# Optimization experiments

Measured on AMD Instinct MI355X. Metric: run time of the kernel, lower is better.

Reference implementation:

```python
import jax, jax.numpy as jnp
import numpy as np

H = 8            # num_heads
EPS = 1e-5       # LayerNorm eps (torch default)
SLOPE = 0.01     # leaky_relu negative slope (torch default)


def layernorm(x, g, b):
    mu = jnp.mean(x, axis=-1, keepdims=True)
    var = jnp.mean((x - mu) ** 2, axis=-1, keepdims=True)
    return (x - mu) * jax.lax.rsqrt(var + EPS) * g + b


def setup_inputs() -> dict:
    key = jax.random.key(0)
    ks = jax.random.split(key, 20)
    B, T, Din, Dh = 4, 2048, 512, 512
    s_in = 1.0 / np.sqrt(Din)
    s_h = 1.0 / np.sqrt(Dh)
    inp = {
        'q': jax.random.normal(ks[0], (B, T, Din), jnp.float32),
        'k': jax.random.normal(ks[1], (B, T, Din), jnp.float32),
        'v': jax.random.normal(ks[2], (B, T, Din), jnp.float32),
        # attention projections (stored as [in, out] for x @ W + b)
        'Wq': jax.random.uniform(ks[3], (Din, Dh), jnp.float32, -s_in, s_in),
        'bq': jax.random.uniform(ks[4], (Dh,), jnp.float32, -s_in, s_in),
        'Wk': jax.random.uniform(ks[5], (Din, Dh), jnp.float32, -s_in, s_in),
        'bk': jax.random.uniform(ks[6], (Dh,), jnp.float32, -s_in, s_in),
        'Wv': jax.random.uniform(ks[7], (Din, Dh), jnp.float32, -s_in, s_in),
        'bv': jax.random.uniform(ks[8], (Dh,), jnp.float32, -s_in, s_in),
        'Wo': jax.random.uniform(ks[9], (Dh, Dh), jnp.float32, -s_h, s_h),
        'bo': jax.random.uniform(ks[10], (Dh,), jnp.float32, -s_h, s_h),
        # FFN
        'Wh': jax.random.uniform(ks[11], (Dh, Dh), jnp.float32, -s_h, s_h),
        'bh': jax.random.uniform(ks[12], (Dh,), jnp.float32, -s_h, s_h),
        'W2': jax.random.uniform(ks[13], (Dh, Dh), jnp.float32, -s_h, s_h),
        'b2': jax.random.uniform(ks[14], (Dh,), jnp.float32, -s_h, s_h),
        # LayerNorms
        'g1': jnp.ones((Dh,), jnp.float32),
        'be1': jnp.zeros((Dh,), jnp.float32),
        'g2': jnp.ones((Dh,), jnp.float32),
        'be2': jnp.zeros((Dh,), jnp.float32),
    }
    return inp


def _block(q, k, v, Wq, bq, Wk, bk, Wv, bv, Wo, bo, Wh, bh, W2, b2, g1, be1, g2, be2):
    B, Tq, _ = q.shape
    Tk = k.shape[1]
    Dh = Wq.shape[1]
    dh = Dh // H
    # projections -> [B, H, T, dh]
    qh = (q @ Wq + bq).reshape(B, Tq, H, dh).transpose(0, 2, 1, 3)
    kh = (k @ Wk + bk).reshape(B, Tk, H, dh).transpose(0, 2, 1, 3)
    vh = (v @ Wv + bv).reshape(B, Tk, H, dh).transpose(0, 2, 1, 3)
    scores = jnp.einsum('bhqd,bhkd->bhqk', qh, kh) / np.sqrt(dh)
    # causal mask: tril with diagonal = Tk - Tq (matches get_causal_mask)
    mask = jnp.tril(jnp.ones((Tq, Tk), bool), k=Tk - Tq)
    scores = jnp.where(mask, scores, -jnp.inf)
    attn = jax.nn.softmax(scores, axis=-1)
    x = jnp.einsum('bhqk,bhkd->bhqd', attn, vh)
    x = x.transpose(0, 2, 1, 3).reshape(B, Tq, Dh)
    h = x @ Wo + bo
    if h.shape == q.shape:
        h = h + q  # residual
    h = layernorm(h, g1, be1)
    y = jax.nn.leaky_relu(h @ Wh + bh, SLOPE) @ W2 + b2
    y = y + h  # residual (shapes always equal here)
    return layernorm(y, g2, be2)


def reference(q, k, v, Wq, bq, Wk, bk, Wv, bv, Wo, bo, Wh, bh, W2, b2, g1, be1, g2, be2):
    return _block(q, k, v, Wq, bq, Wk, bk, Wv, bv, Wo, bo, Wh, bh, W2, b2, g1, be1, g2, be2)
```

## Files before the change

kernel.cpp:

```cpp
#include <hip/hip_runtime.h>
#include <math.h>

#define DIN   512
#define TSEQ  2048
#define BATCH 4
#define NH    8
#define DHEAD 64
#define MTOT  8192

typedef __attribute__((ext_vector_type(8))) __bf16 bf16x8;
typedef __attribute__((ext_vector_type(8))) short  s16x8;
typedef __attribute__((ext_vector_type(4))) float  f32x4;

__device__ __forceinline__ unsigned short f2b(float f) {
  union { float f; unsigned int u; } c; c.f = f;
  unsigned int r = (c.u + 0x7fffu + ((c.u >> 16) & 1u)) >> 16;
  return (unsigned short)r;
}

__device__ __forceinline__ unsigned int pkbf(float a, float b) {
  union { __bf16 h[2]; unsigned int u; } c;
  c.h[0] = (__bf16)a; c.h[1] = (__bf16)b; return c.u;
}

__device__ __forceinline__ f32x4 mfma16(bf16x8 a, bf16x8 b, f32x4 c) {
  return __builtin_amdgcn_mfma_f32_16x16x32_bf16(a, b, c, 0, 0, 0);
}

__device__ __forceinline__ void gload16(const void* gsrc, void* ldsbase) {
  __builtin_amdgcn_global_load_lds(
      (const __attribute__((address_space(1))) unsigned int*)gsrc,
      (__attribute__((address_space(3))) unsigned int*)(unsigned int)(unsigned long long)ldsbase,
      16, 0, 0);
}

#define VMCNT0_BARRIER() do { \
    asm volatile("s_waitcnt vmcnt(0)" ::: "memory"); \
    __builtin_amdgcn_s_barrier(); } while (0)

__global__ __launch_bounds__(256) void cast3_kernel(const float* __restrict__ q,
                                                    const float* __restrict__ k,
                                                    const float* __restrict__ v,
                                                    unsigned short* __restrict__ oq,
                                                    unsigned short* __restrict__ ok,
                                                    unsigned short* __restrict__ ov) {
  const float* in = blockIdx.y == 0 ? q : blockIdx.y == 1 ? k : v;
  unsigned short* out = blockIdx.y == 0 ? oq : blockIdx.y == 1 ? ok : ov;
  int i = (blockIdx.x * 256 + threadIdx.x) * 8;
  float4 a = *(const float4*)(in + i);
  float4 b = *(const float4*)(in + i + 4);
  ushort4 u0, u1;
  u0.x = f2b(a.x); u0.y = f2b(a.y); u0.z = f2b(a.z); u0.w = f2b(a.w);
  u1.x = f2b(b.x); u1.y = f2b(b.y); u1.z = f2b(b.z); u1.w = f2b(b.w);
  *(ushort4*)(out + i) = u0;
  *(ushort4*)(out + i + 4) = u1;
}

__global__ __launch_bounds__(256) void transpose6_kernel(const float* __restrict__ w0,
                                                         const float* __restrict__ w1,
                                                         const float* __restrict__ w2,
                                                         const float* __restrict__ w3,
                                                         const float* __restrict__ w4,
                                                         const float* __restrict__ w5,
                                                         unsigned short* __restrict__ Wt) {
  const float* W;
  switch (blockIdx.z) {
    case 0: W = w0; break; case 1: W = w1; break; case 2: W = w2; break;
    case 3: W = w3; break; case 4: W = w4; break; default: W = w5; break;
  }
  unsigned short* dst = Wt + (size_t)blockIdx.z * 512 * 512;
  __shared__ float tile[32][33];
  int bx = blockIdx.x * 32, by = blockIdx.y * 32;
  int tx = threadIdx.x & 31, ty = threadIdx.x >> 5;
  #pragma unroll
  for (int yy = ty; yy < 32; yy += 8)
    tile[yy][tx] = W[(size_t)(by + yy) * DIN + bx + tx];
  __syncthreads();
  #pragma unroll
  for (int yy = ty; yy < 32; yy += 8)
    dst[(size_t)(bx + yy) * DIN + by + tx] = f2b(tile[tx][yy]);
}

__device__ __forceinline__ void gemm_core(const unsigned short* __restrict__ A,
                                          const unsigned short* __restrict__ Bt,
                                          int m0, int n0,
                                          unsigned short (*Als)[64 * 64],
                                          unsigned short (*Bls)[128 * 64],
                                          f32x4 (*acc)[4]) {
  const int tid = threadIdx.x, lane = tid & 63, w = tid >> 6;
  const int wr = w >> 1, wc = w & 1;
  const int l = lane & 15, g = lane >> 4;
  const int r8 = lane >> 3;
  const int sce = ((lane & 7) ^ r8) * 8;
  const int sxr = (l & 7) * 8;

  #define GSTAGE(buf, k0) do { \
      _Pragma("unroll") \
      for (int i_ = 0; i_ < 2; ++i_) { \
        int ia_ = w * 2 + i_; \
        gload16(A + (size_t)(m0 + ia_ * 8 + r8) * 512 + (k0) + sce, &Als[buf][ia_ * 512]); \
      } \
      _Pragma("unroll") \
      for (int i_ = 0; i_ < 4; ++i_) { \
        int ib_ = w * 4 + i_; \
        gload16(Bt + (size_t)(n0 + ib_ * 8 + r8) * 512 + (k0) + sce, &Bls[buf][ib_ * 512]); \
      } } while (0)

  GSTAGE(0, 0);
  VMCNT0_BARRIER();
  for (int t = 0; t < 8; ++t) {
    int cur = t & 1;
    if (t < 7) GSTAGE(cur ^ 1, (t + 1) * 64);
    #pragma unroll
    for (int kk = 0; kk < 2; ++kk) {
      bf16x8 af[2], bf[4];
      #pragma unroll
      for (int m = 0; m < 2; ++m)
        af[m] = *(const bf16x8*)(&Als[cur][(wr * 32 + m * 16 + l) * 64 + ((kk * 32 + g * 8) ^ sxr)]);
      #pragma unroll
      for (int n = 0; n < 4; ++n)
        bf[n] = *(const bf16x8*)(&Bls[cur][(wc * 64 + n * 16 + l) * 64 + ((kk * 32 + g * 8) ^ sxr)]);
      #pragma unroll
      for (int m = 0; m < 2; ++m)
        #pragma unroll
        for (int n = 0; n < 4; ++n)
          acc[m][n] = mfma16(af[m], bf[n], acc[m][n]);
    }
    VMCNT0_BARRIER();
  }
  #undef GSTAGE
}

enum { EPI_BF16 = 0, EPI_F32RES = 2, EPI_LRELU = 3 };

template <int EPI>
__global__ __launch_bounds__(256) void gemm_kernel(const unsigned short* __restrict__ A,
                                                   const unsigned short* __restrict__ Bt,
                                                   const float* __restrict__ bias,
                                                   const float* __restrict__ res,
                                                   void* __restrict__ out) {
  __shared__ unsigned short Als[2][64 * 64];
  __shared__ unsigned short Bls[2][128 * 64];
  const int lane = threadIdx.x & 63, w = threadIdx.x >> 6;
  const int wr = w >> 1, wc = w & 1;
  const int l = lane & 15, g = lane >> 4;
  const int m0 = blockIdx.x * 64, n0 = blockIdx.y * 128;
  f32x4 acc[2][4] = {};
  gemm_core(A, Bt, m0, n0, Als, Bls, acc);

  #pragma unroll
  for (int m = 0; m < 2; ++m) {
    int grb = m0 + wr * 32 + m * 16 + g * 4;
    #pragma unroll
    for (int n = 0; n < 4; ++n) {
      int gc = n0 + wc * 64 + n * 16 + l;
      float bv = bias[gc];
      #pragma unroll
      for (int r = 0; r < 4; ++r) {
        int gr = grb + r;
        float v = acc[m][n][r] + bv;
        if (EPI == EPI_F32RES) {
          ((float*)out)[(size_t)gr * 512 + gc] = v + res[(size_t)gr * 512 + gc];
        } else if (EPI == EPI_BF16) {
          ((unsigned short*)out)[(size_t)gr * 512 + gc] = f2b(v);
        } else {
          v = v > 0.f ? v : 0.01f * v;
          ((unsigned short*)out)[(size_t)gr * 512 + gc] = f2b(v);
        }
      }
    }
  }
}

__global__ __launch_bounds__(256) void gemm_qkv_kernel(const unsigned short* __restrict__ qb,
                                                       const unsigned short* __restrict__ kb,
                                                       const unsigned short* __restrict__ vb,
                                                       const unsigned short* __restrict__ Wt,
                                                       const float* __restrict__ bq,
                                                       const float* __restrict__ bk,
                                                       const float* __restrict__ bv,
                                                       unsigned short* __restrict__ Qp,
                                                       unsigned short* __restrict__ Kp,
                                                       unsigned short* __restrict__ Vt) {
  __shared__ unsigned short Als[2][64 * 64];
  __shared__ unsigned short Bls[2][128 * 64];
  const int z = blockIdx.z;
  const unsigned short* A = z == 0 ? qb : z == 1 ? kb : vb;
  const unsigned short* B = Wt + (size_t)z * 512 * 512;
  const float* bias = z == 0 ? bq : z == 1 ? bk : bv;
  const int lane = threadIdx.x & 63, w = threadIdx.x >> 6;
  const int wr = w >> 1, wc = w & 1;
  const int l = lane & 15, g = lane >> 4;
  const int m0 = blockIdx.x * 64, n0 = blockIdx.y * 128;
  f32x4 acc[2][4] = {};
  gemm_core(A, B, m0, n0, Als, Bls, acc);

  #pragma unroll
  for (int m = 0; m < 2; ++m) {
    int grb = m0 + wr * 32 + m * 16 + g * 4;
    #pragma unroll
    for (int n = 0; n < 4; ++n) {
      int gc = n0 + wc * 64 + n * 16 + l;
      float bvl = bias[gc];
      #pragma unroll
      for (int r = 0; r < 4; ++r) {
        int gr = grb + r;
        float v = acc[m][n][r] + bvl;
        if (z == 0) {
          Qp[(size_t)gr * 512 + gc] = f2b(v);
        } else if (z == 1) {
          Kp[(size_t)gr * 512 + gc] = f2b(v);
        } else {
          int b = gr >> 11, t = gr & 2047;
          Vt[((size_t)(b * 512 + gc) << 11) + t] = f2b(v);
        }
      }
    }
  }
}

__global__ __launch_bounds__(256) void attn_kernel(const unsigned short* __restrict__ Q,
                                                   const unsigned short* __restrict__ K,
                                                   const unsigned short* __restrict__ Vt,
                                                   unsigned short* __restrict__ O) {
  __shared__ unsigned short Kls[2][64 * 64];
  __shared__ unsigned short Vls[2][64 * 64];
  __shared__ unsigned short Pls[4][16 * 64];
  const int tid = threadIdx.x, lane = tid & 63, w = tid >> 6;
  const int l = lane & 15, g = lane >> 4;
  const int j = blockIdx.x;
  const int bh = blockIdx.y;
  const int b = bh >> 3, h = bh & 7;
  const int sx = (l & 7) * 8;
  const int n1 = 32 - j;
  const float SC2 = 0.125f * 1.44269504088896340736f;
  const float THR = 64.f;

  const int r8 = lane >> 3;
  const int sce = ((lane & 7) ^ r8) * 8;

  #define STAGEKV(buf, kv0) do { \
      _Pragma("unroll") \
      for (int i_ = 0; i_ < 2; ++i_) { \
        int ii_ = w * 2 + i_; \
        int row_ = ii_ * 8 + r8; \
        gload16(K  + (size_t)(b * 2048 + (kv0) + row_) * 512 + h * 64 + sce, &Kls[buf][ii_ * 512]); \
        gload16(Vt + (size_t)(b * 512 + h * 64 + row_) * 2048 + (kv0) + sce, &Vls[buf][ii_ * 512]); \
      } } while (0)

  int tile = 31 - j;
  int q0 = tile * 64 + w * 16;
  bf16x8 qf[2];
  #pragma unroll
  for (int kf = 0; kf < 2; ++kf)
    qf[kf] = *(const bf16x8*)(Q + (size_t)(b * 2048 + q0 + l) * 512 + h * 64 + kf * 32 + g * 8);

  float mrun = -1e30f, lrun = 0.f;
  f32x4 o[4] = {};

  STAGEKV(0, 0);
  VMCNT0_BARRIER();

  for (int s = 0; s <= 32; ++s) {
    int cur = s & 1;
    int kb = s < n1 ? s : s - n1;
    int kv0 = kb * 64;
    if (s < 32) {
      int kbn = (s + 1) < n1 ? (s + 1) : (s + 1) - n1;
      STAGEKV(cur ^ 1, kbn * 64);
    }

    f32x4 st[4];
    #pragma unroll
    for (int t = 0; t < 4; ++t) {
      st[t] = f32x4{0.f, 0.f, 0.f, 0.f};
      #pragma unroll
      for (int kf = 0; kf < 2; ++kf) {
        bf16x8 kfr = *(const bf16x8*)(&Kls[cur][(t * 16 + l) * 64 + ((kf * 32 + g * 8) ^ sx)]);
        st[t] = mfma16(kfr, qf[kf], st[t]);
      }
    }
    if (kb == tile) {
      const int qrow = q0 + l;
      #pragma unroll
      for (int t = 0; t < 4; ++t)
        #pragma unroll
        for (int r = 0; r < 4; ++r)
          if (kv0 + t * 16 + g * 4 + r > qrow) st[t][r] = -1e30f;
    }

    float mx = fmaxf(fmaxf(fmaxf(st[0][0], st[0][1]), fmaxf(st[0][2], st[0][3])),
                     fmaxf(fmaxf(st[1][0], st[1][1]), fmaxf(st[1][2], st[1][3])));
    mx = fmaxf(mx, fmaxf(fmaxf(fmaxf(st[2][0], st[2][1]), fmaxf(st[2][2], st[2][3])),
                         fmaxf(fmaxf(st[3][0], st[3][1]), fmaxf(st[3][2], st[3][3]))));
    mx = fmaxf(mx, __shfl_xor(mx, 16, 64));
    mx = fmaxf(mx, __shfl_xor(mx, 32, 64));

    if (!__all(mx <= mrun + THR)) {
      float nm = fmaxf(mrun, mx);
      float alpha = exp2f((mrun - nm) * SC2);
      mrun = nm;
      lrun *= alpha;
      #pragma unroll
      for (int r = 0; r < 4; ++r) {
        float ar = __shfl(alpha, g * 4 + r, 64);
        #pragma unroll
        for (int n = 0; n < 4; ++n) o[n][r] *= ar;
      }
    }

    float mS = mrun * SC2;
    float rs = 0.f;
    #pragma unroll
    for (int t = 0; t < 4; ++t)
      #pragma unroll
      for (int r = 0; r < 4; ++r) {
        float p = exp2f(fmaf(st[t][r], SC2, -mS));
        st[t][r] = p;
        rs += p;
      }
    rs += __shfl_xor(rs, 16, 64);
    rs += __shfl_xor(rs, 32, 64);
    lrun += rs;

    #pragma unroll
    for (int t = 0; t < 4; ++t) {
      uint2 u;
      u.x = pkbf(st[t][0], st[t][1]);
      u.y = pkbf(st[t][2], st[t][3]);
      *(uint2*)(&Pls[w][l * 64 + ((t * 16 + g * 4) ^ sx)]) = u;
    }
    #pragma unroll
    for (int kf = 0; kf < 2; ++kf) {
      bf16x8 pa = *(const bf16x8*)(&Pls[w][l * 64 + ((kf * 32 + g * 8) ^ sx)]);
      #pragma unroll
      for (int n = 0; n < 4; ++n) {
        bf16x8 vf = *(const bf16x8*)(&Vls[cur][(n * 16 + l) * 64 + ((kf * 32 + g * 8) ^ sx)]);
        o[n] = mfma16(pa, vf, o[n]);
      }
    }

    if (s == n1 - 1) {
      float li = 1.f / lrun;
      #pragma unroll
      for (int r = 0; r < 4; ++r) {
        float lir = __shfl(li, g * 4 + r, 64);
        #pragma unroll
        for (int n = 0; n < 4; ++n)
          O[(size_t)(b * 2048 + q0 + g * 4 + r) * 512 + h * 64 + n * 16 + l] =
              f2b(o[n][r] * lir);
      }
      tile = j;
      q0 = tile * 64 + w * 16;
      #pragma unroll
      for (int kf = 0; kf < 2; ++kf)
        qf[kf] = *(const bf16x8*)(Q + (size_t)(b * 2048 + q0 + l) * 512 + h * 64 + kf * 32 + g * 8);
      mrun = -1e30f; lrun = 0.f;
      #pragma unroll
      for (int n = 0; n < 4; ++n) o[n] = f32x4{0.f, 0.f, 0.f, 0.f};
    }
    VMCNT0_BARRIER();
  }

  float li = 1.f / lrun;
  #pragma unroll
  for (int r = 0; r < 4; ++r) {
    float lir = __shfl(li, g * 4 + r, 64);
    #pragma unroll
    for (int n = 0; n < 4; ++n)
      O[(size_t)(b * 2048 + q0 + g * 4 + r) * 512 + h * 64 + n * 16 + l] =
          f2b(o[n][r] * lir);
  }
  #undef STAGEKV
}

template <int WRITE_BF16>
__global__ __launch_bounds__(256) void ln_kernel(const float* __restrict__ X,
                                                 const float* __restrict__ g,
                                                 const float* __restrict__ be,
                                                 float* __restrict__ Yf,
                                                 unsigned short* __restrict__ Yb) {
  int row = blockIdx.x * 4 + (threadIdx.x >> 6);
  int lane = threadIdx.x & 63;
  const float* x = X + (size_t)row * 512;
  float4 v0 = *(const float4*)(x + lane * 4);
  float4 v1 = *(const float4*)(x + 256 + lane * 4);
  float s = v0.x + v0.y + v0.z + v0.w + v1.x + v1.y + v1.z + v1.w;
  #pragma unroll
  for (int t = 1; t < 64; t <<= 1) s += __shfl_xor(s, t, 64);
  float mu = s * (1.f / 512.f);
  float q = 0.f;
  q += (v0.x - mu) * (v0.x - mu); q += (v0.y - mu) * (v0.y - mu);
  q += (v0.z - mu) * (v0.z - mu); q += (v0.w - mu) * (v0.w - mu);
  q += (v1.x - mu) * (v1.x - mu); q += (v1.y - mu) * (v1.y - mu);
  q += (v1.z - mu) * (v1.z - mu); q += (v1.w - mu) * (v1.w - mu);
  #pragma unroll
  for (int t = 1; t < 64; t <<= 1) q += __shfl_xor(q, t, 64);
  float rstd = rsqrtf(q * (1.f / 512.f) + 1e-5f);

  float4 g0 = *(const float4*)(g + lane * 4);
  float4 g1 = *(const float4*)(g + 256 + lane * 4);
  float4 b0 = *(const float4*)(be + lane * 4);
  float4 b1 = *(const float4*)(be + 256 + lane * 4);
  float4 y0, y1;
  y0.x = (v0.x - mu) * rstd * g0.x + b0.x; y0.y = (v0.y - mu) * rstd * g0.y + b0.y;
  y0.z = (v0.z - mu) * rstd * g0.z + b0.z; y0.w = (v0.w - mu) * rstd * g0.w + b0.w;
  y1.x = (v1.x - mu) * rstd * g1.x + b1.x; y1.y = (v1.y - mu) * rstd * g1.y + b1.y;
  y1.z = (v1.z - mu) * rstd * g1.z + b1.z; y1.w = (v1.w - mu) * rstd * g1.w + b1.w;
  if (Yf) {
    *(float4*)(Yf + (size_t)row * 512 + lane * 4) = y0;
    *(float4*)(Yf + (size_t)row * 512 + 256 + lane * 4) = y1;
  }
  if (WRITE_BF16) {
    ushort4 u0, u1;
    u0.x = f2b(y0.x); u0.y = f2b(y0.y); u0.z = f2b(y0.z); u0.w = f2b(y0.w);
    u1.x = f2b(y1.x); u1.y = f2b(y1.y); u1.z = f2b(y1.z); u1.w = f2b(y1.w);
    *(ushort4*)(Yb + (size_t)row * 512 + lane * 4) = u0;
    *(ushort4*)(Yb + (size_t)row * 512 + 256 + lane * 4) = u1;
  }
}

extern "C" void kernel_launch(void* const* d_in, const int* in_sizes, int n_in,
                              void* d_out, int out_size, void* d_ws, size_t ws_size,
                              hipStream_t stream) {
  const float* q_in = (const float*)d_in[0];
  const float* k_in = (const float*)d_in[1];
  const float* v_in = (const float*)d_in[2];
  const float* Wq = (const float*)d_in[3];  const float* bq = (const float*)d_in[4];
  const float* Wk = (const float*)d_in[5];  const float* bk = (const float*)d_in[6];
  const float* Wv = (const float*)d_in[7];  const float* bv = (const float*)d_in[8];
  const float* Wo = (const float*)d_in[9];  const float* bo = (const float*)d_in[10];
  const float* Wh = (const float*)d_in[11]; const float* bh = (const float*)d_in[12];
  const float* W2 = (const float*)d_in[13]; const float* b2 = (const float*)d_in[14];
  const float* g1 = (const float*)d_in[15]; const float* be1 = (const float*)d_in[16];
  const float* g2 = (const float*)d_in[17]; const float* be2 = (const float*)d_in[18];

  char* ws = (char*)d_ws;
  const size_t MD2 = (size_t)MTOT * 512 * 2;
  const size_t W1  = (size_t)512 * 512 * 2;
  const size_t MD4 = (size_t)MTOT * 512 * 4;
  unsigned short* qb_  = (unsigned short*)(ws);
  unsigned short* kb_  = (unsigned short*)(ws + MD2);
  unsigned short* vb_  = (unsigned short*)(ws + 2 * MD2);
  unsigned short* Qp   = (unsigned short*)(ws + 3 * MD2);
  unsigned short* Kp   = (unsigned short*)(ws + 4 * MD2);
  unsigned short* Vt   = (unsigned short*)(ws + 5 * MD2);
  unsigned short* Wt   = (unsigned short*)(ws + 6 * MD2);
  float*          hy   = (float*)(ws + 6 * MD2 + 6 * W1);
  float*          ln1f = (float*)(ws + 6 * MD2 + 6 * W1 + MD4);
  unsigned short* attn = vb_;
  unsigned short* ln1b = qb_;
  unsigned short* f1   = kb_;

  cast3_kernel<<<dim3(MTOT * 512 / 2048, 3), 256, 0, stream>>>(q_in, k_in, v_in, qb_, kb_, vb_);
  transpose6_kernel<<<dim3(16, 16, 6), 256, 0, stream>>>(Wq, Wk, Wv, Wo, Wh, W2, Wt);

  gemm_qkv_kernel<<<dim3(MTOT / 64, 4, 3), 256, 0, stream>>>(
      qb_, kb_, vb_, Wt, bq, bk, bv, Qp, Kp, Vt);

  attn_kernel<<<dim3(16, BATCH * NH), 256, 0, stream>>>(Qp, Kp, Vt, attn);

  dim3 gg(MTOT / 64, 4);
  gemm_kernel<EPI_F32RES><<<gg, 256, 0, stream>>>(attn, Wt + 3 * 512 * 512, bo, q_in, hy);
  ln_kernel<1><<<MTOT / 4, 256, 0, stream>>>(hy, g1, be1, ln1f, ln1b);
  gemm_kernel<EPI_LRELU><<<gg, 256, 0, stream>>>(ln1b, Wt + 4 * 512 * 512, bh, nullptr, f1);
  gemm_kernel<EPI_F32RES><<<gg, 256, 0, stream>>>(f1, Wt + 5 * 512 * 512, b2, ln1f, hy);
  ln_kernel<0><<<MTOT / 4, 256, 0, stream>>>(hy, g2, be2, (float*)d_out, nullptr);
}
```

Baseline: 258.9 us.

## Triple-buffer LDS staging with vmcnt-based waits in GEMM and attention kernels

```diff
diff --git a/kernel.cpp b/kernel.cpp
--- a/kernel.cpp
+++ b/kernel.cpp
@@ -34,9 +34,7 @@
       16, 0, 0);
 }
 
-#define VMCNT0_BARRIER() do { \
-    asm volatile("s_waitcnt vmcnt(0)" ::: "memory"); \
-    __builtin_amdgcn_s_barrier(); } while (0)
+#define WAITV(N) asm volatile("s_waitcnt vmcnt(" #N ")" ::: "memory")
 
 __global__ __launch_bounds__(256) void cast3_kernel(const float* __restrict__ q,
                                                     const float* __restrict__ k,
@@ -107,10 +105,15 @@
       } } while (0)
 
   GSTAGE(0, 0);
-  VMCNT0_BARRIER();
+  GSTAGE(1, 64);
+  int cur = 0;
   for (int t = 0; t < 8; ++t) {
-    int cur = t & 1;
-    if (t < 7) GSTAGE(cur ^ 1, (t + 1) * 64);
+    if (t < 7) { WAITV(6); } else { WAITV(0); }
+    __builtin_amdgcn_s_barrier();
+    if (t < 6) {
+      int nb = cur + 2; if (nb >= 3) nb -= 3;
+      GSTAGE(nb, (t + 2) * 64);
+    }
     #pragma unroll
     for (int kk = 0; kk < 2; ++kk) {
       bf16x8 af[2], bf[4];
@@ -126,7 +129,7 @@
         for (int n = 0; n < 4; ++n)
           acc[m][n] = mfma16(af[m], bf[n], acc[m][n]);
     }
-    VMCNT0_BARRIER();
+    cur = cur == 2 ? 0 : cur + 1;
   }
   #undef GSTAGE
 }
@@ -139,8 +142,8 @@
                                                    const float* __restrict__ bias,
                                                    const float* __restrict__ res,
                                                    void* __restrict__ out) {
-  __shared__ unsigned short Als[2][64 * 64];
-  __shared__ unsigned short Bls[2][128 * 64];
+  __shared__ unsigned short Als[3][64 * 64];
+  __shared__ unsigned short Bls[3][128 * 64];
   const int lane = threadIdx.x & 63, w = threadIdx.x >> 6;
   const int wr = w >> 1, wc = w & 1;
   const int l = lane & 15, g = lane >> 4;
@@ -182,8 +185,8 @@
                                                        unsigned short* __restrict__ Qp,
                                                        unsigned short* __restrict__ Kp,
                                                        unsigned short* __restrict__ Vt) {
-  __shared__ unsigned short Als[2][64 * 64];
-  __shared__ unsigned short Bls[2][128 * 64];
+  __shared__ unsigned short Als[3][64 * 64];
+  __shared__ unsigned short Bls[3][128 * 64];
   const int z = blockIdx.z;
   const unsigned short* A = z == 0 ? qb : z == 1 ? kb : vb;
   const unsigned short* B = Wt + (size_t)z * 512 * 512;
@@ -223,13 +226,13 @@
                                                    const unsigned short* __restrict__ K,
                                                    const unsigned short* __restrict__ Vt,
                                                    unsigned short* __restrict__ O) {
-  __shared__ unsigned short Kls[2][64 * 64];
-  __shared__ unsigned short Vls[2][64 * 64];
+  __shared__ unsigned short Kls[3][64 * 64];
+  __shared__ unsigned short Vls[3][64 * 64];
   __shared__ unsigned short Pls[4][16 * 64];
   const int tid = threadIdx.x, lane = tid & 63, w = tid >> 6;
   const int l = lane & 15, g = lane >> 4;
-  const int j = blockIdx.x;
-  const int bh = blockIdx.y;
+  const int j = blockIdx.y;
+  const int bh = blockIdx.x;
   const int b = bh >> 3, h = bh & 7;
   const int sx = (l & 7) * 8;
   const int n1 = 32 - j;
@@ -259,16 +262,20 @@
   f32x4 o[4] = {};
 
   STAGEKV(0, 0);
-  VMCNT0_BARRIER();
+  STAGEKV(1, 64);
+  int cur = 0;
 
   for (int s = 0; s <= 32; ++s) {
-    int cur = s & 1;
+    if (s < 32) { WAITV(4); } else { WAITV(0); }
+    __builtin_amdgcn_s_barrier();
+    if (s + 2 <= 32) {
+      int sp = s + 2;
+      int kbp = sp < n1 ? sp : sp - n1;
+      int nb = cur + 2; if (nb >= 3) nb -= 3;
+      STAGEKV(nb, kbp * 64);
+    }
     int kb = s < n1 ? s : s - n1;
     int kv0 = kb * 64;
-    if (s < 32) {
-      int kbn = (s + 1) < n1 ? (s + 1) : (s + 1) - n1;
-      STAGEKV(cur ^ 1, kbn * 64);
-    }
 
     f32x4 st[4];
     #pragma unroll
@@ -359,7 +366,7 @@
       #pragma unroll
       for (int n = 0; n < 4; ++n) o[n] = f32x4{0.f, 0.f, 0.f, 0.f};
     }
-    VMCNT0_BARRIER();
+    cur = cur == 2 ? 0 : cur + 1;
   }
 
   float li = 1.f / lrun;
@@ -458,7 +465,7 @@
   gemm_qkv_kernel<<<dim3(MTOT / 64, 4, 3), 256, 0, stream>>>(
       qb_, kb_, vb_, Wt, bq, bk, bv, Qp, Kp, Vt);
 
-  attn_kernel<<<dim3(16, BATCH * NH), 256, 0, stream>>>(Qp, Kp, Vt, attn);
+  attn_kernel<<<dim3(BATCH * NH, 16), 256, 0, stream>>>(Qp, Kp, Vt, attn);
 
   dim3 gg(MTOT / 64, 4);
   gemm_kernel<EPI_F32RES><<<gg, 256, 0, stream>>>(attn, Wt + 3 * 512 * 512, bo, q_in, hy);
```

After: 256.1 us. No clear change (-1.1%).

## Launch one attention block per query tile and compute softmax row sums via MFMA

Applied to the files above, without the earlier changes.

```diff
diff --git a/kernel.cpp b/kernel.cpp
--- a/kernel.cpp
+++ b/kernel.cpp
@@ -228,11 +228,10 @@
   __shared__ unsigned short Pls[4][16 * 64];
   const int tid = threadIdx.x, lane = tid & 63, w = tid >> 6;
   const int l = lane & 15, g = lane >> 4;
-  const int j = blockIdx.x;
-  const int bh = blockIdx.y;
+  const int bh = blockIdx.x;
+  const int qt = (int)gridDim.y - 1 - (int)blockIdx.y;
   const int b = bh >> 3, h = bh & 7;
   const int sx = (l & 7) * 8;
-  const int n1 = 32 - j;
   const float SC2 = 0.125f * 1.44269504088896340736f;
   const float THR = 64.f;
 
@@ -248,27 +247,27 @@
         gload16(Vt + (size_t)(b * 512 + h * 64 + row_) * 2048 + (kv0) + sce, &Vls[buf][ii_ * 512]); \
       } } while (0)
 
-  int tile = 31 - j;
-  int q0 = tile * 64 + w * 16;
+  const int q0 = qt * 64 + w * 16;
   bf16x8 qf[2];
   #pragma unroll
   for (int kf = 0; kf < 2; ++kf)
     qf[kf] = *(const bf16x8*)(Q + (size_t)(b * 2048 + q0 + l) * 512 + h * 64 + kf * 32 + g * 8);
 
-  float mrun = -1e30f, lrun = 0.f;
+  bf16x8 vones;
+  #pragma unroll
+  for (int i = 0; i < 8; ++i) vones[i] = (__bf16)1.0f;
+
+  float mrun = -1e30f;
   f32x4 o[4] = {};
+  f32x4 os = {0.f, 0.f, 0.f, 0.f};
 
   STAGEKV(0, 0);
   VMCNT0_BARRIER();
 
-  for (int s = 0; s <= 32; ++s) {
+  for (int s = 0; s <= qt; ++s) {
     int cur = s & 1;
-    int kb = s < n1 ? s : s - n1;
-    int kv0 = kb * 64;
-    if (s < 32) {
-      int kbn = (s + 1) < n1 ? (s + 1) : (s + 1) - n1;
-      STAGEKV(cur ^ 1, kbn * 64);
-    }
+    if (s < qt) STAGEKV(cur ^ 1, (s + 1) * 64);
+    int kv0 = s * 64;
 
     f32x4 st[4];
     #pragma unroll
@@ -280,7 +279,7 @@
         st[t] = mfma16(kfr, qf[kf], st[t]);
       }
     }
-    if (kb == tile) {
+    if (s == qt) {
       const int qrow = q0 + l;
       #pragma unroll
       for (int t = 0; t < 4; ++t)
@@ -289,10 +288,12 @@
           if (kv0 + t * 16 + g * 4 + r > qrow) st[t][r] = -1e30f;
     }
 
-    float mx = fmaxf(fmaxf(fmaxf(st[0][0], st[0][1]), fmaxf(st[0][2], st[0][3])),
-                     fmaxf(fmaxf(st[1][0], st[1][1]), fmaxf(st[1][2], st[1][3])));
-    mx = fmaxf(mx, fmaxf(fmaxf(fmaxf(st[2][0], st[2][1]), fmaxf(st[2][2], st[2][3])),
-                         fmaxf(fmaxf(st[3][0], st[3][1]), fmaxf(st[3][2], st[3][3]))));
+    float mx = fmaxf(
+        fmaxf(fmaxf(fmaxf(st[0][0], st[0][1]), st[0][2]),
+              fmaxf(fmaxf(st[0][3], st[1][0]), st[1][1])),
+        fmaxf(fmaxf(fmaxf(st[1][2], st[1][3]), st[2][0]),
+              fmaxf(fmaxf(st[2][1], st[2][2]), st[2][3])));
+    mx = fmaxf(mx, fmaxf(fmaxf(st[3][0], st[3][1]), fmaxf(st[3][2], st[3][3])));
     mx = fmaxf(mx, __shfl_xor(mx, 16, 64));
     mx = fmaxf(mx, __shfl_xor(mx, 32, 64));
 
@@ -300,28 +301,21 @@
       float nm = fmaxf(mrun, mx);
       float alpha = exp2f((mrun - nm) * SC2);
       mrun = nm;
-      lrun *= alpha;
       #pragma unroll
       for (int r = 0; r < 4; ++r) {
         float ar = __shfl(alpha, g * 4 + r, 64);
         #pragma unroll
         for (int n = 0; n < 4; ++n) o[n][r] *= ar;
+        os[r] *= ar;
       }
     }
 
     float mS = mrun * SC2;
-    float rs = 0.f;
     #pragma unroll
     for (int t = 0; t < 4; ++t)
       #pragma unroll
-      for (int r = 0; r < 4; ++r) {
-        float p = exp2f(fmaf(st[t][r], SC2, -mS));
-        st[t][r] = p;
-        rs += p;
-      }
-    rs += __shfl_xor(rs, 16, 64);
-    rs += __shfl_xor(rs, 32, 64);
-    lrun += rs;
+      for (int r = 0; r < 4; ++r)
+        st[t][r] = exp2f(fmaf(st[t][r], SC2, -mS));
 
     #pragma unroll
     for (int t = 0; t < 4; ++t) {
@@ -338,34 +332,15 @@
         bf16x8 vf = *(const bf16x8*)(&Vls[cur][(n * 16 + l) * 64 + ((kf * 32 + g * 8) ^ sx)]);
         o[n] = mfma16(pa, vf, o[n]);
       }
-    }
-
-    if (s == n1 - 1) {
-      float li = 1.f / lrun;
-      #pragma unroll
-      for (int r = 0; r < 4; ++r) {
-        float lir = __shfl(li, g * 4 + r, 64);
-        #pragma unroll
-        for (int n = 0; n < 4; ++n)
-          O[(size_t)(b * 2048 + q0 + g * 4 + r) * 512 + h * 64 + n * 16 + l] =
-              f2b(o[n][r] * lir);
-      }
-      tile = j;
-      q0 = tile * 64 + w * 16;
-      #pragma unroll
-      for (int kf = 0; kf < 2; ++kf)
-        qf[kf] = *(const bf16x8*)(Q + (size_t)(b * 2048 + q0 + l) * 512 + h * 64 + kf * 32 + g * 8);
-      mrun = -1e30f; lrun = 0.f;
-      #pragma unroll
-      for (int n = 0; n < 4; ++n) o[n] = f32x4{0.f, 0.f, 0.f, 0.f};
-    }
+      os = mfma16(pa, vones, os);
+    }
+
     VMCNT0_BARRIER();
   }
 
-  float li = 1.f / lrun;
   #pragma unroll
   for (int r = 0; r < 4; ++r) {
-    float lir = __shfl(li, g * 4 + r, 64);
+    float lir = 1.f / os[r];
     #pragma unroll
     for (int n = 0; n < 4; ++n)
       O[(size_t)(b * 2048 + q0 + g * 4 + r) * 512 + h * 64 + n * 16 + l] =
@@ -458,7 +433,7 @@
   gemm_qkv_kernel<<<dim3(MTOT / 64, 4, 3), 256, 0, stream>>>(
       qb_, kb_, vb_, Wt, bq, bk, bv, Qp, Kp, Vt);
 
-  attn_kernel<<<dim3(16, BATCH * NH), 256, 0, stream>>>(Qp, Kp, Vt, attn);
+  attn_kernel<<<dim3(BATCH * NH, 32), 256, 0, stream>>>(Qp, Kp, Vt, attn);
 
   dim3 gg(MTOT / 64, 4);
   gemm_kernel<EPI_F32RES><<<gg, 256, 0, stream>>>(attn, Wt + 3 * 512 * 512, bo, q_in, hy);
```

New measurement: 255.9 us. About the same (-1.2%).
